# Optimization experiments

Hardware: AMD Instinct MI355X
Metric: run time of the kernel (lower is better)

The kernel has to match this reference:

```python
import jax, jax.numpy as jnp
import numpy as np

B, T1, T2, C, H, NIN = 4, 4096, 2048, 512, 8, 3
D = C // H  # head_dim = 64


def setup_inputs() -> dict:
    key = jax.random.key(0)
    ks = jax.random.split(key, 10)
    s = 0.02  # weight init scale
    return {
        "x": jax.random.normal(ks[0], (B, T1, C), jnp.float32),
        "y0": jax.random.normal(ks[1], (B, T2, C), jnp.float32),
        "y1": jax.random.normal(ks[2], (B, T2, C), jnp.float32),
        "y2": jax.random.normal(ks[3], (B, T2, C), jnp.float32),
        "Wq": jax.random.normal(ks[4], (C, C), jnp.float32) * s,
        "bq": jnp.zeros((C,), jnp.float32),
        "Wk": jax.random.normal(ks[5], (NIN, C, C), jnp.float32) * s,
        "bk": jnp.zeros((NIN, C), jnp.float32),
        "Wv": jax.random.normal(ks[6], (NIN, C, C), jnp.float32) * s,
        "bv": jnp.zeros((NIN, C), jnp.float32),
        "Wo": jax.random.normal(ks[7], (C, C), jnp.float32) * s,
        "bo": jnp.zeros((C,), jnp.float32),
    }


def _heads(t, n_head):
    b, n, c = t.shape
    return t.reshape(b, n, n_head, c // n_head).transpose(0, 2, 1, 3)  # [B,H,N,D]


def reference(x, y0, y1, y2, Wq, bq, Wk, bk, Wv, bv, Wo, bo):
    b, t1, c = x.shape
    q = jax.nn.softmax(_heads(x @ Wq.T + bq, H), axis=-1)  # [B,H,T1,D]
    out = q  # note: original initializes accumulator with q itself
    for i, y in enumerate((y0, y1, y2)):
        k = jax.nn.softmax(_heads(y @ Wk[i].T + bk[i], H), axis=-1)  # [B,H,T2,D]
        v = _heads(y @ Wv[i].T + bv[i], H)                            # [B,H,T2,D]
        k_sum = k.sum(axis=-2, keepdims=True)                         # [B,H,1,D]
        D_inv = 1.0 / ((q * k_sum).sum(axis=-1, keepdims=True) + 1e-8)  # [B,H,T1,1]
        context = jnp.einsum('bhnd,bhnv->bhdv', k, v)                 # [B,H,D,D]
        out = out + jnp.einsum('bhqd,bhdv->bhqv', q, context) * D_inv
    out = out.transpose(0, 2, 1, 3).reshape(b, t1, c)
    return out @ Wo.T + bo
```

## Files before the change

kernel.cpp:

```cpp
#include <hip/hip_runtime.h>
#include <stdint.h>

#define B_ 4
#define T1_ 4096
#define T2_ 2048
#define C_ 512
#define H_ 8
#define D_ 64
#define M1_ (B_*T1_)
#define M2_ (B_*T2_)

using f32x4 = __attribute__((ext_vector_type(4))) float;
using bf16x8 = __attribute__((ext_vector_type(8))) __bf16;
using us8 = __attribute__((ext_vector_type(8))) unsigned short;
using us4 = __attribute__((ext_vector_type(4))) unsigned short;

__device__ __forceinline__ unsigned short f2bf(float f){
  unsigned int u = __builtin_bit_cast(unsigned int, f);
  unsigned int r = (u + 0x7fffu + ((u >> 16) & 1u)) >> 16;
  return (unsigned short)r;
}
__device__ __forceinline__ float bf2f(unsigned short u){
  return __builtin_bit_cast(float, ((unsigned int)u) << 16);
}
__device__ __forceinline__ f32x4 mfma16(us8 a, us8 b, f32x4 c){
  return __builtin_amdgcn_mfma_f32_16x16x32_bf16(
      __builtin_bit_cast(bf16x8, a), __builtin_bit_cast(bf16x8, b), c, 0, 0, 0);
}
__device__ __forceinline__ us8 cvt8(f32x4 a, f32x4 b){
  us8 v;
  #pragma unroll
  for (int j = 0; j < 4; ++j){
    v[j]   = __builtin_bit_cast(unsigned short, (__bf16)a[j]);
    v[4+j] = __builtin_bit_cast(unsigned short, (__bf16)b[j]);
  }
  return v;
}

typedef const __attribute__((address_space(1))) unsigned int gu32;
typedef __attribute__((address_space(3))) unsigned int lu32;
__device__ __forceinline__ void gl_lds16(const void* g, void* l){
  __builtin_amdgcn_global_load_lds((gu32*)g, (lu32*)l, 16, 0, 0);
}

#define WAIT_VM(N) asm volatile("s_waitcnt vmcnt(" #N ")" ::: "memory")
#define RAW_BAR()  { __builtin_amdgcn_s_barrier(); __builtin_amdgcn_sched_barrier(0); }

__device__ __forceinline__ int swz(int row, int blk){ return blk ^ ((row >> 1) & 3); }

__global__ __launch_bounds__(256) void cvt_bf16_4(const float* __restrict__ p0, const float* __restrict__ p1,
                                                  const float* __restrict__ p2, const float* __restrict__ p3,
                                                  unsigned short* o0, unsigned short* o1,
                                                  unsigned short* o2, unsigned short* o3,
                                                  int n0, int n1, int n2, int n3){
  const float* in; unsigned short* out; int n4;
  switch (blockIdx.y){
    case 0: in = p0; out = o0; n4 = n0; break;
    case 1: in = p1; out = o1; n4 = n1; break;
    case 2: in = p2; out = o2; n4 = n2; break;
    default: in = p3; out = o3; n4 = n3; break;
  }
  int i = blockIdx.x * 256 + threadIdx.x;
  if (i >= n4) return;
  f32x4 v = ((const f32x4*)in)[i];
  us4 o;
  #pragma unroll
  for (int j = 0; j < 4; ++j) o[j] = f2bf(v[j]);
  ((us4*)out)[i] = o;
}

__device__ __forceinline__ void tile_write(unsigned short* tile, const f32x4 (&vals)[4][4],
                                           int wr, int wc, int lr, int lk){
  #pragma unroll
  for (int mt = 0; mt < 4; ++mt)
    #pragma unroll
    for (int nt = 0; nt < 4; ++nt)
      #pragma unroll
      for (int r = 0; r < 4; ++r){
        int row = wr*64 + mt*16 + lk*4 + r;
        int cb  = (wc*128 + nt*32 + lr*2) ^ ((row & 7) << 4);
        *(unsigned short*)((char*)tile + row*256 + cb) = f2bf(vals[mt][nt][r]);
      }
}
__device__ __forceinline__ void tile_write_T(unsigned short* tile, const f32x4 (&vals)[4][4],
                                             int wr, int wc, int lr, int lk){
  #pragma unroll
  for (int mt = 0; mt < 4; ++mt)
    #pragma unroll
    for (int nt = 0; nt < 4; ++nt)
      #pragma unroll
      for (int r = 0; r < 4; ++r){
        int n  = wr*64 + mt*16 + lk*4 + r;
        int ch = wc*64 + nt*16 + lr;
        int cb = (n*2) ^ ((ch & 7) << 4);
        *(unsigned short*)((char*)tile + ch*256 + cb) = f2bf(vals[mt][nt][r]);
      }
}
__device__ __forceinline__ void tile_flush(const unsigned short* tile, unsigned short* g,
                                           size_t row0, int col0, int ldg, int t){
  #pragma unroll
  for (int p = 0; p < 8; ++p){
    int row = p*16 + (t >> 4);
    int cb  = ((t & 15) * 16) ^ ((row & 7) << 4);
    us8 v = *(const us8*)((const char*)tile + row*256 + cb);
    *(us8*)(g + (row0 + row) * (size_t)ldg + col0 + (t & 15) * 8) = v;
  }
}

__global__ __launch_bounds__(256) void proj(const float* __restrict__ xf,
                                            const float* __restrict__ y0f,
                                            const float* __restrict__ y1f,
                                            const float* __restrict__ y2f,
                                            const unsigned short* __restrict__ wqb,
                                            const unsigned short* __restrict__ wkb,
                                            const unsigned short* __restrict__ wvb,
                                            const float* __restrict__ bq,
                                            const float* __restrict__ bk,
                                            const float* __restrict__ bv,
                                            unsigned short* __restrict__ qb,
                                            unsigned short* __restrict__ kbT,
                                            unsigned short* __restrict__ vbT,
                                            float* __restrict__ ksum){
  __shared__ unsigned short smem[36864];
  const int hw = blockIdx.x;
  const int work = (hw & 7) * 256 + (hw >> 3);
  int seg, ii, m0, n0;
  const float* Af;
  const unsigned short* W;
  const float* bias;
  if (work < 512){
    seg = 0; ii = 0;
    m0 = (work >> 2) << 7; n0 = (work & 3) << 7;
    Af = xf; W = wqb; bias = bq;
  } else {
    int r = work - 512;
    int g = r >> 3, s = r & 7;
    ii = g >> 6; m0 = (g & 63) << 7;
    seg = (s < 4) ? 1 : 2;
    n0 = (s & 3) << 7;
    Af = (ii == 0) ? y0f : (ii == 1 ? y1f : y2f);
    W = (seg == 1 ? wkb : wvb) + (size_t)ii*C_*C_;
    bias = (seg == 1 ? bk : bv) + (size_t)ii*C_;
  }
  const int t = threadIdx.x;
  const int w = t >> 6, l = t & 63;
  const int wr = w >> 1, wc = w & 1;
  const int lr = l & 15, lk = l >> 4;
  f32x4 acc[4][4] = {};

#define STAGE(BB, TT) { \
    _Pragma("unroll") \
    for (int j = 0; j < 4; ++j){ \
      int c = t + j*256, row = c >> 3, ch = c & 7; \
      gl_lds16(Af + (size_t)(m0+row)*C_ + (TT)*32 + ((ch ^ (row & 7)) << 2), \
               &smem[(BB)*8192 + c*8]); \
    } \
    { int c = t, row = c >> 2; \
      gl_lds16(W + (size_t)(n0+row)*C_ + (TT)*32 + swz(row, c & 3)*8, &smem[24576 + (BB)*4096 + c*8]); \
      c = t + 256; row = c >> 2; \
      gl_lds16(W + (size_t)(n0+row)*C_ + (TT)*32 + swz(row, c & 3)*8, &smem[24576 + (BB)*4096 + c*8]); } }
#define PCOMP(BB) { \
    const float* sAf = (const float*)&smem[(BB)*8192]; \
    const unsigned short* sW = &smem[24576 + (BB)*4096]; \
    us8 af[4], bfr[4]; \
    _Pragma("unroll") \
    for (int mt = 0; mt < 4; ++mt){ \
      int R = wr*64 + mt*16 + lr, x = R & 7; \
      f32x4 a0 = *(const f32x4*)(sAf + R*32 + (((2*lk)     ^ x) << 2)); \
      f32x4 a1 = *(const f32x4*)(sAf + R*32 + (((2*lk + 1) ^ x) << 2)); \
      af[mt] = cvt8(a0, a1); \
    } \
    _Pragma("unroll") \
    for (int nt = 0; nt < 4; ++nt){ int R = wc*64 + nt*16 + lr; bfr[nt] = *(const us8*)&sW[R*32 + swz(R, lk)*8]; } \
    __builtin_amdgcn_s_setprio(1); \
    _Pragma("unroll") \
    for (int mt = 0; mt < 4; ++mt) \
      _Pragma("unroll") \
      for (int nt = 0; nt < 4; ++nt) \
        acc[mt][nt] = mfma16(af[mt], bfr[nt], acc[mt][nt]); \
    __builtin_amdgcn_s_setprio(0); }

  STAGE(0, 0);
  int cur = 0;
  #pragma unroll 1
  for (int tt = 0; tt < 15; ++tt){
    int nxt = (cur == 2) ? 0 : cur + 1;
    STAGE(nxt, tt + 1);
    WAIT_VM(6);
    RAW_BAR();
    PCOMP(cur);
    cur = nxt;
  }
  WAIT_VM(0);
  RAW_BAR();
  PCOMP(cur);
#undef STAGE
#undef PCOMP

  {
    float bc[4];
    #pragma unroll
    for (int nt = 0; nt < 4; ++nt) bc[nt] = bias[n0 + wc*64 + nt*16 + lr];
    #pragma unroll
    for (int mt = 0; mt < 4; ++mt)
      #pragma unroll
      for (int nt = 0; nt < 4; ++nt)
        #pragma unroll
        for (int r = 0; r < 4; ++r) acc[mt][nt][r] += bc[nt];
  }
  if (seg <= 1){
    #pragma unroll
    for (int mt = 0; mt < 4; ++mt)
      #pragma unroll
      for (int r = 0; r < 4; ++r){
        float m = fmaxf(fmaxf(acc[mt][0][r], acc[mt][1][r]), fmaxf(acc[mt][2][r], acc[mt][3][r]));
        #pragma unroll
        for (int s = 1; s < 16; s <<= 1) m = fmaxf(m, __shfl_xor(m, s, 64));
        float sum = 0.f;
        #pragma unroll
        for (int nt = 0; nt < 4; ++nt){
          float e = __expf(acc[mt][nt][r] - m);
          acc[mt][nt][r] = e; sum += e;
        }
        #pragma unroll
        for (int s = 1; s < 16; s <<= 1) sum += __shfl_xor(sum, s, 64);
        float inv = 1.0f / sum;
        #pragma unroll
        for (int nt = 0; nt < 4; ++nt) acc[mt][nt][r] *= inv;
      }
  }
  if (seg == 1){
    const int b = m0 >> 11;
    #pragma unroll
    for (int nt = 0; nt < 4; ++nt){
      float cs = 0.f;
      #pragma unroll
      for (int mt = 0; mt < 4; ++mt)
        #pragma unroll
        for (int r = 0; r < 4; ++r) cs += acc[mt][nt][r];
      cs += __shfl_xor(cs, 16, 64);
      cs += __shfl_xor(cs, 32, 64);
      if (lk == 0)
        atomicAdd(&ksum[((size_t)ii*B_ + b)*C_ + n0 + wc*64 + nt*16 + lr], cs);
    }
  }
  __syncthreads();
  if (seg == 0){
    tile_write(smem, acc, wr, wc, lr, lk);
    __syncthreads();
    tile_flush(smem, qb, m0, n0, C_, t);
  } else {
    tile_write_T(smem, acc, wr, wc, lr, lk);
    __syncthreads();
    const int b = m0 >> 11;
    const int n_base = m0 & 2047;
    unsigned short* gT = (seg == 1 ? kbT : vbT);
    tile_flush(smem, gT, ((size_t)ii*B_ + b)*C_ + n0, n_base, T2_, t);
  }
}

__global__ __launch_bounds__(256) void ctx_mfma(const unsigned short* __restrict__ kbT,
                                                const unsigned short* __restrict__ vbT,
                                                float* __restrict__ part){
  const int bh = blockIdx.x, kc = blockIdx.y, i = blockIdx.z;
  const int b = bh >> 3, h = bh & 7;
  const size_t rowbase = ((size_t)i*B_ + b)*C_ + h*64;
  const unsigned short* kT = kbT + rowbase*T2_;
  const unsigned short* vT = vbT + rowbase*T2_;
  const int t = threadIdx.x;
  const int w = t >> 6, l = t & 63;
  const int qr = w >> 1, qc = w & 1;
  const int lr = l & 15, lk = l >> 4;
  const int n00 = kc * 256;
  f32x4 acc[2][2] = {};
  #pragma unroll
  for (int it = 0; it < 8; ++it){
    const int k0 = n00 + it*32 + lk*8;
    us8 a0 = *(const us8*)(kT + (size_t)(qr*32 +      lr)*T2_ + k0);
    us8 a1 = *(const us8*)(kT + (size_t)(qr*32 + 16 + lr)*T2_ + k0);
    us8 b0 = *(const us8*)(vT + (size_t)(qc*32 +      lr)*T2_ + k0);
    us8 b1 = *(const us8*)(vT + (size_t)(qc*32 + 16 + lr)*T2_ + k0);
    acc[0][0] = mfma16(a0, b0, acc[0][0]);
    acc[0][1] = mfma16(a0, b1, acc[0][1]);
    acc[1][0] = mfma16(a1, b0, acc[1][0]);
    acc[1][1] = mfma16(a1, b1, acc[1][1]);
  }
  float* dst = part + (((size_t)i*8 + kc)*32 + bh)*4096;
  #pragma unroll
  for (int fa = 0; fa < 2; ++fa)
    #pragma unroll
    for (int fb = 0; fb < 2; ++fb){
      int d0 = qr*32 + fa*16 + lk*4;
      int e  = qc*32 + fb*16 + lr;
      *(f32x4*)(dst + e*64 + d0) = acc[fa][fb];
    }
}

__global__ __launch_bounds__(256) void ctx_reduce(const float* __restrict__ part,
                                                  unsigned short* __restrict__ ctxTb){
  const int bh = blockIdx.x, i = blockIdx.y, t = threadIdx.x;
  for (int idx = t; idx < 4096; idx += 256){
    float s = 0.f;
    #pragma unroll
    for (int kc = 0; kc < 8; ++kc)
      s += part[(((size_t)i*8 + kc)*32 + bh)*4096 + idx];
    ctxTb[((size_t)i*32 + bh)*4096 + idx] = f2bf(s);
  }
}

__global__ __launch_bounds__(256) void combine(const unsigned short* __restrict__ qb,
                                               const unsigned short* __restrict__ ctxTb,
                                               const float* __restrict__ ksum,
                                               unsigned short* __restrict__ omid){
  __shared__ unsigned short tile[128*128];
  const int hw = blockIdx.x;
  const int work = (hw & 7) * 64 + (hw >> 3);
  const int m0 = (work & 127) << 7, n0 = (work >> 7) << 7;
  const int t = threadIdx.x;
  const int w = t >> 6, l = t & 63;
  const int wr = w >> 1, wc = w & 1;
  const int lr = l & 15, lk = l >> 4;
  const int b = m0 >> 12;
  const int bh = b*8 + (n0 >> 6) + wc;
  #pragma unroll
  for (int p = 0; p < 8; ++p){
    int idx = p*256 + t;
    int row = idx >> 4, ch = idx & 15;
    gl_lds16(qb + (size_t)(m0+row)*C_ + n0 + (ch ^ (row & 7))*8, &tile[idx*8]);
  }
  WAIT_VM(0);
  __syncthreads();
  us8 afr[4][2];
  #pragma unroll
  for (int mt = 0; mt < 4; ++mt)
    #pragma unroll
    for (int kk = 0; kk < 2; ++kk){
      int row = wr*64 + mt*16 + lr;
      int ch = wc*8 + kk*4 + lk;
      afr[mt][kk] = *(const us8*)((const char*)tile + row*256 + ((ch ^ (row & 7)) << 4));
    }
  f32x4 acc[4][4];
  #pragma unroll
  for (int mt = 0; mt < 4; ++mt)
    #pragma unroll
    for (int nt = 0; nt < 4; ++nt)
      #pragma unroll
      for (int r = 0; r < 4; ++r){
        int row = wr*64 + mt*16 + lk*4 + r;
        int cbyte = wc*128 + nt*32 + lr*2;
        int ch = cbyte >> 4;
        unsigned short v = *(const unsigned short*)((const char*)tile + row*256 +
                            ((ch ^ (row & 7)) << 4) + (cbyte & 15));
        acc[mt][nt][r] = bf2f(v);
      }
  us8 bden[2];
  #pragma unroll
  for (int kk = 0; kk < 2; ++kk){
    us8 tmp = {};
    if (lr < 3){
      const float* kp = ksum + ((size_t)lr*B_ + b)*C_ + n0 + wc*64 + kk*32 + lk*8;
      f32x4 c0 = *(const f32x4*)kp;
      f32x4 c1 = *(const f32x4*)(kp + 4);
      #pragma unroll
      for (int j = 0; j < 4; ++j){ tmp[j] = f2bf(c0[j]); tmp[4+j] = f2bf(c1[j]); }
    }
    bden[kk] = tmp;
  }
  f32x4 den[4] = {};
  #pragma unroll
  for (int mt = 0; mt < 4; ++mt)
    #pragma unroll
    for (int kk = 0; kk < 2; ++kk)
      den[mt] = mfma16(afr[mt][kk], bden[kk], den[mt]);
  #pragma unroll 1
  for (int i = 0; i < 3; ++i){
    f32x4 dinv[4];
    #pragma unroll
    for (int mt = 0; mt < 4; ++mt)
      #pragma unroll
      for (int r = 0; r < 4; ++r)
        dinv[mt][r] = 1.0f / (__shfl(den[mt][r], (l & 48) | i, 64) + 1e-8f);
    #pragma unroll
    for (int nt = 0; nt < 4; ++nt){
      us8 bfr[2];
      #pragma unroll
      for (int kk = 0; kk < 2; ++kk)
        bfr[kk] = *(const us8*)(ctxTb + ((size_t)(i*32 + bh))*4096 + (nt*16 + lr)*64 + kk*32 + lk*8);
      f32x4 p[4] = {};
      #pragma unroll
      for (int mt = 0; mt < 4; ++mt)
        #pragma unroll
        for (int kk = 0; kk < 2; ++kk)
          p[mt] = mfma16(afr[mt][kk], bfr[kk], p[mt]);
      #pragma unroll
      for (int mt = 0; mt < 4; ++mt)
        #pragma unroll
        for (int r = 0; r < 4; ++r)
          acc[mt][nt][r] += p[mt][r] * dinv[mt][r];
    }
  }
  __syncthreads();
  tile_write(tile, acc, wr, wc, lr, lk);
  __syncthreads();
  tile_flush(tile, omid, m0, n0, C_, t);
}

__global__ __launch_bounds__(256, 3) void gemm_bt(const unsigned short* __restrict__ A,
                                                  const unsigned short* __restrict__ Bw,
                                                  const float* __restrict__ bias,
                                                  float* __restrict__ out){
  __shared__ unsigned short smem[3*2*4096];
  const int hw = blockIdx.x;
  const int work = (hw & 7) * 64 + (hw >> 3);
  const int m0 = ((work >> 2) & 127) << 7, n0 = (work & 3) << 7;
  const int t = threadIdx.x;
  const int w = t >> 6, l = t & 63;
  const int wr = w >> 1, wc = w & 1;
  const int lr = l & 15, lk = l >> 4;
  f32x4 acc[4][4] = {};

#define GSTAGE(BB, TT) { \
    int c = t, row = c >> 2; \
    gl_lds16(A  + (size_t)(m0+row)*C_ + (TT)*32 + swz(row, c & 3)*8, &smem[(BB)*8192 + c*8]); \
    gl_lds16(Bw + (size_t)(n0+row)*C_ + (TT)*32 + swz(row, c & 3)*8, &smem[(BB)*8192 + 4096 + c*8]); \
    c = t + 256; row = c >> 2; \
    gl_lds16(A  + (size_t)(m0+row)*C_ + (TT)*32 + swz(row, c & 3)*8, &smem[(BB)*8192 + c*8]); \
    gl_lds16(Bw + (size_t)(n0+row)*C_ + (TT)*32 + swz(row, c & 3)*8, &smem[(BB)*8192 + 4096 + c*8]); }
#define GCOMP(BB) { \
    const unsigned short* sA = &smem[(BB)*8192]; \
    const unsigned short* sB = &smem[(BB)*8192 + 4096]; \
    us8 af[4], bfr[4]; \
    _Pragma("unroll") \
    for (int mt = 0; mt < 4; ++mt){ int R = wr*64 + mt*16 + lr; af[mt] = *(const us8*)&sA[R*32 + swz(R, lk)*8]; } \
    _Pragma("unroll") \
    for (int nt = 0; nt < 4; ++nt){ int R = wc*64 + nt*16 + lr; bfr[nt] = *(const us8*)&sB[R*32 + swz(R, lk)*8]; } \
    __builtin_amdgcn_s_setprio(1); \
    _Pragma("unroll") \
    for (int mt = 0; mt < 4; ++mt) \
      _Pragma("unroll") \
      for (int nt = 0; nt < 4; ++nt) \
        acc[mt][nt] = mfma16(af[mt], bfr[nt], acc[mt][nt]); \
    __builtin_amdgcn_s_setprio(0); }
#define GSTEP(T, N) { \
    if ((T) + 2 < 16) GSTAGE(((T)+2)%3, (T)+2); \
    WAIT_VM(N); \
    RAW_BAR(); \
    GCOMP((T)%3); }

  GSTAGE(0, 0); GSTAGE(1, 1);
  GSTEP(0, 8)  GSTEP(1, 8)  GSTEP(2, 8)  GSTEP(3, 8)
  GSTEP(4, 8)  GSTEP(5, 8)  GSTEP(6, 8)  GSTEP(7, 8)
  GSTEP(8, 8)  GSTEP(9, 8)  GSTEP(10, 8) GSTEP(11, 8)
  GSTEP(12, 8) GSTEP(13, 8) GSTEP(14, 4) GSTEP(15, 0)
#undef GSTAGE
#undef GCOMP
#undef GSTEP

  #pragma unroll
  for (int mt = 0; mt < 4; ++mt)
    #pragma unroll
    for (int nt = 0; nt < 4; ++nt)
      #pragma unroll
      for (int r = 0; r < 4; ++r){
        int row = m0 + wr*64 + mt*16 + lk*4 + r;
        int col = n0 + wc*64 + nt*16 + lr;
        out[(size_t)row*C_ + col] = acc[mt][nt][r] + bias[col];
      }
}

extern "C" void kernel_launch(void* const* d_in, const int* in_sizes, int n_in,
                              void* d_out, int out_size, void* d_ws, size_t ws_size,
                              hipStream_t stream){
  const float* x  = (const float*)d_in[0];
  const float* y0 = (const float*)d_in[1];
  const float* y1 = (const float*)d_in[2];
  const float* y2 = (const float*)d_in[3];
  const float* Wq = (const float*)d_in[4];
  const float* bq = (const float*)d_in[5];
  const float* Wk = (const float*)d_in[6];
  const float* bk = (const float*)d_in[7];
  const float* Wv = (const float*)d_in[8];
  const float* bv = (const float*)d_in[9];
  const float* Wo = (const float*)d_in[10];
  const float* bo = (const float*)d_in[11];

  char* ws = (char*)d_ws;
  size_t off = 0;
  auto alloc = [&](size_t bytes)->char*{
    char* p = ws + off; off += (bytes + 1023) & ~((size_t)1023); return p;
  };
  unsigned short* wqb   = (unsigned short*)alloc((size_t)C_*C_*2);
  unsigned short* wkb   = (unsigned short*)alloc((size_t)3*C_*C_*2);
  unsigned short* wvb   = (unsigned short*)alloc((size_t)3*C_*C_*2);
  unsigned short* wob   = (unsigned short*)alloc((size_t)C_*C_*2);
  unsigned short* qb    = (unsigned short*)alloc((size_t)M1_*C_*2);
  unsigned short* kbT   = (unsigned short*)alloc((size_t)3*B_*C_*T2_*2);
  unsigned short* vbT   = (unsigned short*)alloc((size_t)3*B_*C_*T2_*2);
  float*          ksum  = (float*)alloc((size_t)3*B_*C_*4);
  float*          part  = (float*)alloc((size_t)3*8*32*4096*4);
  unsigned short* ctxTb = (unsigned short*)alloc((size_t)3*32*4096*2);
  unsigned short* omid  = (unsigned short*)alloc((size_t)M1_*C_*2);

  (void)hipMemsetAsync(ksum, 0, (size_t)3*B_*C_*4, stream);

  cvt_bf16_4<<<dim3(3*C_*C_/4/256, 4), 256, 0, stream>>>(
      Wq, Wk, Wv, Wo, wqb, wkb, wvb, wob,
      C_*C_/4, 3*C_*C_/4, 3*C_*C_/4, C_*C_/4);

  proj<<<2048, 256, 0, stream>>>(x, y0, y1, y2, wqb, wkb, wvb, bq, bk, bv, qb, kbT, vbT, ksum);
  ctx_mfma<<<dim3(32, 8, 3), 256, 0, stream>>>(kbT, vbT, part);
  ctx_reduce<<<dim3(32, 3), 256, 0, stream>>>(part, ctxTb);
  combine<<<512, 256, 0, stream>>>(qb, ctxTb, ksum, omid);
  gemm_bt<<<512, 256, 0, stream>>>(omid, wob, bo, (float*)d_out);
}
```

Measured before the change: 140.5 us.

## Pre-convert activations to bf16 and restage proj/gemm pipelines after barrier

Adds a separate conversion pass that turns x and y0..y2 from fp32 into bf16 workspace buffers. The projection kernel then loads bf16 tiles, which shrinks its LDS footprint and drops the in-loop fp32-to-bf16 conversion. Its prologue/loop is rewritten as a fully unrolled 3-stage pipeline that issues the next stage after the barrier, with launch bounds raised to allow more resident blocks. The same barrier-then-stage reorder and vmcnt changes are applied to the output GEMM. In exchange, the activations now pass through HBM an extra time (fp32 read plus bf16 write and reread), which may cost more than the per-tile conversion it removes.

Result: no change. 140.7 us (+0.2%).

```diff
diff --git a/kernel.cpp b/kernel.cpp
--- a/kernel.cpp
+++ b/kernel.cpp
@@ -26,15 +26,6 @@
 __device__ __forceinline__ f32x4 mfma16(us8 a, us8 b, f32x4 c){
   return __builtin_amdgcn_mfma_f32_16x16x32_bf16(
       __builtin_bit_cast(bf16x8, a), __builtin_bit_cast(bf16x8, b), c, 0, 0, 0);
-}
-__device__ __forceinline__ us8 cvt8(f32x4 a, f32x4 b){
-  us8 v;
-  #pragma unroll
-  for (int j = 0; j < 4; ++j){
-    v[j]   = __builtin_bit_cast(unsigned short, (__bf16)a[j]);
-    v[4+j] = __builtin_bit_cast(unsigned short, (__bf16)b[j]);
-  }
-  return v;
 }
 
 typedef const __attribute__((address_space(1))) unsigned int gu32;
@@ -107,38 +98,35 @@
   }
 }
 
-__global__ __launch_bounds__(256) void proj(const float* __restrict__ xf,
-                                            const float* __restrict__ y0f,
-                                            const float* __restrict__ y1f,
-                                            const float* __restrict__ y2f,
-                                            const unsigned short* __restrict__ wqb,
-                                            const unsigned short* __restrict__ wkb,
-                                            const unsigned short* __restrict__ wvb,
-                                            const float* __restrict__ bq,
-                                            const float* __restrict__ bk,
-                                            const float* __restrict__ bv,
-                                            unsigned short* __restrict__ qb,
-                                            unsigned short* __restrict__ kbT,
-                                            unsigned short* __restrict__ vbT,
-                                            float* __restrict__ ksum){
-  __shared__ unsigned short smem[36864];
+__global__ __launch_bounds__(256, 3) void proj(const unsigned short* __restrict__ xb,
+                                               const unsigned short* __restrict__ yball,
+                                               const unsigned short* __restrict__ wqb,
+                                               const unsigned short* __restrict__ wkb,
+                                               const unsigned short* __restrict__ wvb,
+                                               const float* __restrict__ bq,
+                                               const float* __restrict__ bk,
+                                               const float* __restrict__ bv,
+                                               unsigned short* __restrict__ qb,
+                                               unsigned short* __restrict__ kbT,
+                                               unsigned short* __restrict__ vbT,
+                                               float* __restrict__ ksum){
+  __shared__ unsigned short smem[3*2*4096];
   const int hw = blockIdx.x;
   const int work = (hw & 7) * 256 + (hw >> 3);
   int seg, ii, m0, n0;
-  const float* Af;
-  const unsigned short* W;
+  const unsigned short *A, *W;
   const float* bias;
   if (work < 512){
     seg = 0; ii = 0;
     m0 = (work >> 2) << 7; n0 = (work & 3) << 7;
-    Af = xf; W = wqb; bias = bq;
+    A = xb; W = wqb; bias = bq;
   } else {
     int r = work - 512;
     int g = r >> 3, s = r & 7;
     ii = g >> 6; m0 = (g & 63) << 7;
     seg = (s < 4) ? 1 : 2;
     n0 = (s & 3) << 7;
-    Af = (ii == 0) ? y0f : (ii == 1 ? y1f : y2f);
+    A = yball + (size_t)ii*M2_*C_;
     W = (seg == 1 ? wkb : wvb) + (size_t)ii*C_*C_;
     bias = (seg == 1 ? bk : bv) + (size_t)ii*C_;
   }
@@ -148,28 +136,19 @@
   const int lr = l & 15, lk = l >> 4;
   f32x4 acc[4][4] = {};
 
-#define STAGE(BB, TT) { \
-    _Pragma("unroll") \
-    for (int j = 0; j < 4; ++j){ \
-      int c = t + j*256, row = c >> 3, ch = c & 7; \
-      gl_lds16(Af + (size_t)(m0+row)*C_ + (TT)*32 + ((ch ^ (row & 7)) << 2), \
-               &smem[(BB)*8192 + c*8]); \
-    } \
-    { int c = t, row = c >> 2; \
-      gl_lds16(W + (size_t)(n0+row)*C_ + (TT)*32 + swz(row, c & 3)*8, &smem[24576 + (BB)*4096 + c*8]); \
-      c = t + 256; row = c >> 2; \
-      gl_lds16(W + (size_t)(n0+row)*C_ + (TT)*32 + swz(row, c & 3)*8, &smem[24576 + (BB)*4096 + c*8]); } }
+#define PSTAGE(BB, TT) { \
+    int c = t, row = c >> 2; \
+    gl_lds16(A + (size_t)(m0+row)*C_ + (TT)*32 + swz(row, c & 3)*8, &smem[(BB)*8192 + c*8]); \
+    gl_lds16(W + (size_t)(n0+row)*C_ + (TT)*32 + swz(row, c & 3)*8, &smem[(BB)*8192 + 4096 + c*8]); \
+    c = t + 256; row = c >> 2; \
+    gl_lds16(A + (size_t)(m0+row)*C_ + (TT)*32 + swz(row, c & 3)*8, &smem[(BB)*8192 + c*8]); \
+    gl_lds16(W + (size_t)(n0+row)*C_ + (TT)*32 + swz(row, c & 3)*8, &smem[(BB)*8192 + 4096 + c*8]); }
 #define PCOMP(BB) { \
-    const float* sAf = (const float*)&smem[(BB)*8192]; \
-    const unsigned short* sW = &smem[24576 + (BB)*4096]; \
+    const unsigned short* sA = &smem[(BB)*8192]; \
+    const unsigned short* sW = &smem[(BB)*8192 + 4096]; \
     us8 af[4], bfr[4]; \
     _Pragma("unroll") \
-    for (int mt = 0; mt < 4; ++mt){ \
-      int R = wr*64 + mt*16 + lr, x = R & 7; \
-      f32x4 a0 = *(const f32x4*)(sAf + R*32 + (((2*lk)     ^ x) << 2)); \
-      f32x4 a1 = *(const f32x4*)(sAf + R*32 + (((2*lk + 1) ^ x) << 2)); \
-      af[mt] = cvt8(a0, a1); \
-    } \
+    for (int mt = 0; mt < 4; ++mt){ int R = wr*64 + mt*16 + lr; af[mt] = *(const us8*)&sA[R*32 + swz(R, lk)*8]; } \
     _Pragma("unroll") \
     for (int nt = 0; nt < 4; ++nt){ int R = wc*64 + nt*16 + lr; bfr[nt] = *(const us8*)&sW[R*32 + swz(R, lk)*8]; } \
     __builtin_amdgcn_s_setprio(1); \
@@ -179,23 +158,20 @@
       for (int nt = 0; nt < 4; ++nt) \
         acc[mt][nt] = mfma16(af[mt], bfr[nt], acc[mt][nt]); \
     __builtin_amdgcn_s_setprio(0); }
-
-  STAGE(0, 0);
-  int cur = 0;
-  #pragma unroll 1
-  for (int tt = 0; tt < 15; ++tt){
-    int nxt = (cur == 2) ? 0 : cur + 1;
-    STAGE(nxt, tt + 1);
-    WAIT_VM(6);
-    RAW_BAR();
-    PCOMP(cur);
-    cur = nxt;
-  }
-  WAIT_VM(0);
-  RAW_BAR();
-  PCOMP(cur);
-#undef STAGE
+#define PSTEP(T, N) { \
+    WAIT_VM(N); \
+    RAW_BAR(); \
+    if ((T) + 2 < 16) PSTAGE(((T)+2)%3, (T)+2); \
+    PCOMP((T)%3); }
+
+  PSTAGE(0, 0); PSTAGE(1, 1);
+  PSTEP(0, 4)  PSTEP(1, 4)  PSTEP(2, 4)  PSTEP(3, 4)
+  PSTEP(4, 4)  PSTEP(5, 4)  PSTEP(6, 4)  PSTEP(7, 4)
+  PSTEP(8, 4)  PSTEP(9, 4)  PSTEP(10, 4) PSTEP(11, 4)
+  PSTEP(12, 4) PSTEP(13, 4) PSTEP(14, 4) PSTEP(15, 0)
+#undef PSTAGE
 #undef PCOMP
+#undef PSTEP
 
   {
     float bc[4];
@@ -442,16 +418,16 @@
         acc[mt][nt] = mfma16(af[mt], bfr[nt], acc[mt][nt]); \
     __builtin_amdgcn_s_setprio(0); }
 #define GSTEP(T, N) { \
-    if ((T) + 2 < 16) GSTAGE(((T)+2)%3, (T)+2); \
     WAIT_VM(N); \
     RAW_BAR(); \
+    if ((T) + 2 < 16) GSTAGE(((T)+2)%3, (T)+2); \
     GCOMP((T)%3); }
 
   GSTAGE(0, 0); GSTAGE(1, 1);
-  GSTEP(0, 8)  GSTEP(1, 8)  GSTEP(2, 8)  GSTEP(3, 8)
-  GSTEP(4, 8)  GSTEP(5, 8)  GSTEP(6, 8)  GSTEP(7, 8)
-  GSTEP(8, 8)  GSTEP(9, 8)  GSTEP(10, 8) GSTEP(11, 8)
-  GSTEP(12, 8) GSTEP(13, 8) GSTEP(14, 4) GSTEP(15, 0)
+  GSTEP(0, 4)  GSTEP(1, 4)  GSTEP(2, 4)  GSTEP(3, 4)
+  GSTEP(4, 4)  GSTEP(5, 4)  GSTEP(6, 4)  GSTEP(7, 4)
+  GSTEP(8, 4)  GSTEP(9, 4)  GSTEP(10, 4) GSTEP(11, 4)
+  GSTEP(12, 4) GSTEP(13, 4) GSTEP(14, 4) GSTEP(15, 0)
 #undef GSTAGE
 #undef GCOMP
 #undef GSTEP
@@ -489,6 +465,8 @@
   auto alloc = [&](size_t bytes)->char*{
     char* p = ws + off; off += (bytes + 1023) & ~((size_t)1023); return p;
   };
+  unsigned short* xb    = (unsigned short*)alloc((size_t)M1_*C_*2);
+  unsigned short* yball = (unsigned short*)alloc((size_t)3*M2_*C_*2);
   unsigned short* wqb   = (unsigned short*)alloc((size_t)C_*C_*2);
   unsigned short* wkb   = (unsigned short*)alloc((size_t)3*C_*C_*2);
   unsigned short* wvb   = (unsigned short*)alloc((size_t)3*C_*C_*2);
@@ -503,11 +481,14 @@
 
   (void)hipMemsetAsync(ksum, 0, (size_t)3*B_*C_*4, stream);
 
+  cvt_bf16_4<<<dim3(M1_*C_/4/256, 4), 256, 0, stream>>>(
+      x, y0, y1, y2, xb, yball, yball + (size_t)M2_*C_, yball + (size_t)2*M2_*C_,
+      M1_*C_/4, M2_*C_/4, M2_*C_/4, M2_*C_/4);
   cvt_bf16_4<<<dim3(3*C_*C_/4/256, 4), 256, 0, stream>>>(
       Wq, Wk, Wv, Wo, wqb, wkb, wvb, wob,
       C_*C_/4, 3*C_*C_/4, 3*C_*C_/4, C_*C_/4);
 
-  proj<<<2048, 256, 0, stream>>>(x, y0, y1, y2, wqb, wkb, wvb, bq, bk, bv, qb, kbT, vbT, ksum);
+  proj<<<2048, 256, 0, stream>>>(xb, yball, wqb, wkb, wvb, bq, bk, bv, qb, kbT, vbT, ksum);
   ctx_mfma<<<dim3(32, 8, 3), 256, 0, stream>>>(kbT, vbT, part);
   ctx_reduce<<<dim3(32, 3), 256, 0, stream>>>(part, ctxTb);
   combine<<<512, 256, 0, stream>>>(qb, ctxTb, ksum, omid);
```
